# Optimization experiments

Measured on AMD Instinct MI355X. Metric: run time of the kernel, lower is better.

The kernel has to match this reference:

```python
import jax, jax.numpy as jnp
import numpy as np

N_NODES = 50000
EMBED_DIM = 100
N_RAND_EDGES = 600000
NEG_SLOPE = 0.2  # alpha in the original module


def _build_pairs(n_nodes, n_edges, seed=0):
    """Replicates: neighbors(v) = unique(out_nbrs(v) U in_nbrs(v)) for all v,
    flattened into (seg=v, nbr=u) pair arrays (symmetrized, deduped edge list)."""
    rng = np.random.default_rng(seed)
    src = rng.integers(0, n_nodes, n_edges)
    dst = rng.integers(0, n_nodes, n_edges)
    ring = np.arange(n_nodes)  # guarantee every node has a neighbor
    src = np.concatenate([src, ring])
    dst = np.concatenate([dst, (ring + 1) % n_nodes])
    seg = np.concatenate([src, dst])
    nbr = np.concatenate([dst, src])
    pairs = np.unique(np.stack([seg, nbr], axis=1), axis=0)  # sorted by seg
    return pairs[:, 0].astype(np.int32), pairs[:, 1].astype(np.int32)


def setup_inputs() -> dict:
    key = jax.random.key(0)
    k1, k2 = jax.random.split(key)
    hidden = jax.random.normal(k1, (N_NODES, EMBED_DIM), dtype=jnp.float32)
    # nn.Linear(embed_dim, 1, bias=False) weight, kaiming-uniform-ish scale
    W = jax.random.normal(k2, (EMBED_DIM,), dtype=jnp.float32) / np.sqrt(EMBED_DIM)
    seg_np, nbr_np = _build_pairs(N_NODES, N_RAND_EDGES)
    return {"hidden": hidden, "W": W,
            "seg": jnp.asarray(seg_np), "nbr": jnp.asarray(nbr_np)}


def reference(hidden, W, seg, nbr):
    n = hidden.shape[0]
    h_i = hidden[seg]            # [P, D] center node repeated per neighbor
    h_j = hidden[nbr]            # [P, D] gathered neighbor embeddings
    scores = jnp.einsum('pd,d->p', h_i * h_j, W)           # a(neighbors*hidden)
    scores = jnp.where(scores >= 0, scores, NEG_SLOPE * scores)  # leaky_relu
    # per-node (segment) softmax, numerically stable
    m = jax.ops.segment_max(scores, seg, num_segments=n)
    e = jnp.exp(scores - m[seg])
    z = jax.ops.segment_sum(e, seg, num_segments=n)
    alpha = e / z[seg]                                      # [P]
    out = jax.ops.segment_sum(alpha[:, None] * h_j, seg, num_segments=n)  # [N, D]
    return out
```

## Files before the change

### kernel.cpp

```cpp
#include <hip/hip_runtime.h>
#include <math.h>

#define D 100
#define NEG_SLOPE 0.2f
#define CHUNK 16
#define ROWU 52
#define NPB 2

#define COMPILER_FENCE() asm volatile("" ::: "memory")

typedef _Float16 f16x2 __attribute__((ext_vector_type(2)));
union U32H2 { unsigned int u; f16x2 h; };

__device__ __forceinline__ unsigned int pkh2(float x, float y) {
    U32H2 c; c.h.x = (_Float16)x; c.h.y = (_Float16)y; return c.u;
}

__device__ __forceinline__ float dot2u(unsigned int au, unsigned int xu, float acc) {
#if __has_builtin(__builtin_amdgcn_fdot2)
    U32H2 a, x; a.u = au; x.u = xu;
    return __builtin_amdgcn_fdot2(a.h, x.h, acc, false);
#else
    U32H2 a, x; a.u = au; x.u = xu;
    return acc + (float)a.h.x * (float)x.h.x + (float)a.h.y * (float)x.h.y;
#endif
}

template<int CTRL>
__device__ __forceinline__ float dppf(float x) {
    return __uint_as_float((unsigned)__builtin_amdgcn_update_dpp(
        0, (int)__float_as_uint(x), CTRL, 0xF, 0xF, true));
}
__device__ __forceinline__ float red16_max(float x) {
    x = fmaxf(x, dppf<0xB1>(x));
    x = fmaxf(x, dppf<0x4E>(x));
    x = fmaxf(x, dppf<0x124>(x));
    x = fmaxf(x, dppf<0x128>(x));
    return x;
}
__device__ __forceinline__ float red16_sum(float x) {
    x += dppf<0xB1>(x);
    x += dppf<0x4E>(x);
    x += dppf<0x124>(x);
    x += dppf<0x128>(x);
    return x;
}

__global__ void prep_kernel(const int* __restrict__ seg,
                            int* __restrict__ row_ptr,
                            const float* __restrict__ hidden,
                            unsigned int* __restrict__ hb,
                            int n, int P, int total25)
{
    int t = blockIdx.x * blockDim.x + threadIdx.x;
    if (t < P) {
        int s0 = seg[t];
        if (t == 0)
            for (int v = 0; v <= s0; v++) row_ptr[v] = 0;
        int s1 = (t + 1 < P) ? seg[t + 1] : n;
        for (int v = s0 + 1; v <= s1; v++) row_ptr[v] = t + 1;
    }
    if (t < total25) {
        int node = t / 25, k = t - node * 25;
        float4 f = ((const float4*)hidden)[t];
        *(uint2*)&hb[node * ROWU + 2 * k] =
            make_uint2(pkh2(f.x, f.y), pkh2(f.z, f.w));
    }
}

__launch_bounds__(64 * NPB, 8)
__global__ void gat_agg_kernel(const float* __restrict__ hidden,
                               const float* __restrict__ W,
                               const int* __restrict__ nbr,
                               const int* __restrict__ row_ptr,
                               const unsigned int* __restrict__ hb,
                               float* __restrict__ out,
                               int n, int P)
{
    __shared__ __align__(16) unsigned int s_hwp[NPB][ROWU];
    __shared__ __align__(16) unsigned int s_rows[NPB][CHUNK][ROWU];
    __shared__ __align__(16) float        s_e[NPB][CHUNK];

    const int lane = threadIdx.x & 63;
    const int wid  = threadIdx.x >> 6;
    const int v    = blockIdx.x * NPB + wid;
    if (v >= n) return;

    if (lane < 50) {
        float2 h2 = ((const float2*)(hidden + (long)v * D))[lane];
        float2 w2 = ((const float2*)W)[lane];
        s_hwp[wid][lane] = pkh2(h2.x * w2.x, h2.y * w2.y);
    }
    COMPILER_FENCE();

    const int start = row_ptr[v];
    const int end   = row_ptr[v + 1];

    if (end <= start) {
        if (lane < D / 2)
            ((float2*)(out + (long)v * D))[lane] = make_float2(0.f, 0.f);
        return;
    }

    const int q  = lane >> 4;
    const int jl = lane & 15;
    const int t0 = q * 3;

    const uint4* hwq = ((const uint4*)&s_hwp[wid][0]) + t0;
    const uint4 a0 = hwq[0], a1 = hwq[1], a2 = hwq[2];
    uint2 at = make_uint2(0u, 0u);
    if (q == 0) at = *(const uint2*)&s_hwp[wid][48];

    float m = -INFINITY, z = 0.f;
    float accx = 0.f, accy = 0.f;

    for (int c = start; c < end; c += CHUNK) {
        const int  cnt = min(CHUNK, end - c);
        const bool pv  = jl < cnt;

        const int nbv = pv ? nbr[c + jl] : 0;
        const uint4* row16 = ((const uint4*)hb) + nbv * (ROWU / 4) + t0;

        uint4 x0 = row16[0], x1 = row16[1], x2 = row16[2];
        uint2 xt = make_uint2(0u, 0u);
        if (q == 0) xt = *(const uint2*)&hb[nbv * ROWU + 48];

        float p0 = 0.f, p1 = 0.f, p2 = 0.f, p3 = 0.f;
        p0 = dot2u(a0.x, x0.x, p0);  p1 = dot2u(a0.y, x0.y, p1);
        p2 = dot2u(a0.z, x0.z, p2);  p3 = dot2u(a0.w, x0.w, p3);
        p0 = dot2u(a1.x, x1.x, p0);  p1 = dot2u(a1.y, x1.y, p1);
        p2 = dot2u(a1.z, x1.z, p2);  p3 = dot2u(a1.w, x1.w, p3);
        p0 = dot2u(a2.x, x2.x, p0);  p1 = dot2u(a2.y, x2.y, p1);
        p2 = dot2u(a2.z, x2.z, p2);  p3 = dot2u(a2.w, x2.w, p3);
        if (q == 0) {
            p0 = dot2u(at.x, xt.x, p0);
            p1 = dot2u(at.y, xt.y, p1);
        }

        uint4* dst16 = ((uint4*)&s_rows[wid][jl][0]) + t0;
        dst16[0] = x0; dst16[1] = x1; dst16[2] = x2;
        if (q == 0) *(uint2*)&s_rows[wid][jl][48] = xt;

        float part = (p0 + p1) + (p2 + p3);
        part += __shfl_xor(part, 16, 64);
        part += __shfl_xor(part, 32, 64);
        const float s = pv ? (part >= 0.f ? part : NEG_SLOPE * part)
                           : -INFINITY;

        const float m_new = fmaxf(m, red16_max(s));
        const float scale = __expf(m - m_new);
        const float e     = pv ? __expf(s - m_new) : 0.f;
        z = z * scale + red16_sum(e);
        accx *= scale; accy *= scale;

        if (lane < CHUNK) s_e[wid][lane] = e;
        COMPILER_FENCE();

        const int cnt4 = (cnt + 3) & ~3;
        if (lane < D / 2) {
            for (int j0 = 0; j0 < cnt4; j0 += 4) {
                const float4 ev = *(const float4*)&s_e[wid][j0];
                U32H2 u0, u1, u2, u3;
                u0.u = s_rows[wid][j0    ][lane];
                u1.u = s_rows[wid][j0 + 1][lane];
                u2.u = s_rows[wid][j0 + 2][lane];
                u3.u = s_rows[wid][j0 + 3][lane];
                accx = fmaf((float)u0.h.x, ev.x, accx);
                accy = fmaf((float)u0.h.y, ev.x, accy);
                accx = fmaf((float)u1.h.x, ev.y, accx);
                accy = fmaf((float)u1.h.y, ev.y, accy);
                accx = fmaf((float)u2.h.x, ev.z, accx);
                accy = fmaf((float)u2.h.y, ev.z, accy);
                accx = fmaf((float)u3.h.x, ev.w, accx);
                accy = fmaf((float)u3.h.y, ev.w, accy);
            }
        }
        COMPILER_FENCE();
        m = m_new;
    }

    if (lane < D / 2) {
        const float inv = 1.f / z;
        ((float2*)(out + (long)v * D))[lane] = make_float2(accx * inv, accy * inv);
    }
}

extern "C" void kernel_launch(void* const* d_in, const int* in_sizes, int n_in,
                              void* d_out, int out_size, void* d_ws, size_t ws_size,
                              hipStream_t stream) {
    const float* hidden = (const float*)d_in[0];
    const float* W      = (const float*)d_in[1];
    const int*   seg    = (const int*)d_in[2];
    const int*   nbr    = (const int*)d_in[3];
    float*       out    = (float*)d_out;

    const int Ddim = in_sizes[1];
    const int n    = in_sizes[0] / Ddim;
    const int P    = in_sizes[2];

    int* row_ptr = (int*)d_ws;
    size_t hb_off = (((size_t)(n + 1) * 4) + 255) & ~(size_t)255;
    unsigned int* hb = (unsigned int*)((char*)d_ws + hb_off);

    const int total25 = n * 25;
    const int tmax    = (P > total25) ? P : total25;
    hipLaunchKernelGGL(prep_kernel, dim3((tmax + 255) / 256), dim3(256), 0, stream,
                       seg, row_ptr, hidden, hb, n, P, total25);
    hipLaunchKernelGGL(gat_agg_kernel, dim3((n + NPB - 1) / NPB), dim3(64 * NPB),
                       0, stream, hidden, W, nbr, row_ptr, hb, out, n, P);
}
```

Measured before the change: 128.4 us.

## Accumulate weighted rows in registers per lane instead of staging through LDS

Each lane now keeps 28 per-column register accumulators for its own neighbor slice and multiplies them by its softmax weight directly. This removes the LDS staging of gathered rows and weights and the serial per-chunk accumulation loop. A DPP reduction across the 16 neighbor lanes runs once at the end, and the rescale is skipped when the running max does not change. The cost is higher register pressure (launch bound occupancy lowered from 8 to 6) and a final reduction of 28 values.

```diff
diff --git a/kernel.cpp b/kernel.cpp
--- a/kernel.cpp
+++ b/kernel.cpp
@@ -68,7 +68,19 @@
     }
 }
 
-__launch_bounds__(64 * NPB, 8)
+#define ACCU4(b, X) do {                                                      \
+    U32H2 t_;                                                                 \
+    t_.u = (X).x; accA[(b)+0] = fmaf((float)t_.h.x, e, accA[(b)+0]);          \
+                  accA[(b)+1] = fmaf((float)t_.h.y, e, accA[(b)+1]);          \
+    t_.u = (X).y; accA[(b)+2] = fmaf((float)t_.h.x, e, accA[(b)+2]);          \
+                  accA[(b)+3] = fmaf((float)t_.h.y, e, accA[(b)+3]);          \
+    t_.u = (X).z; accA[(b)+4] = fmaf((float)t_.h.x, e, accA[(b)+4]);          \
+                  accA[(b)+5] = fmaf((float)t_.h.y, e, accA[(b)+5]);          \
+    t_.u = (X).w; accA[(b)+6] = fmaf((float)t_.h.x, e, accA[(b)+6]);          \
+                  accA[(b)+7] = fmaf((float)t_.h.y, e, accA[(b)+7]);          \
+} while (0)
+
+__launch_bounds__(64 * NPB, 6)
 __global__ void gat_agg_kernel(const float* __restrict__ hidden,
                                const float* __restrict__ W,
                                const int* __restrict__ nbr,
@@ -78,8 +90,6 @@
                                int n, int P)
 {
     __shared__ __align__(16) unsigned int s_hwp[NPB][ROWU];
-    __shared__ __align__(16) unsigned int s_rows[NPB][CHUNK][ROWU];
-    __shared__ __align__(16) float        s_e[NPB][CHUNK];
 
     const int lane = threadIdx.x & 63;
     const int wid  = threadIdx.x >> 6;
@@ -111,8 +121,14 @@
     uint2 at = make_uint2(0u, 0u);
     if (q == 0) at = *(const uint2*)&s_hwp[wid][48];
 
+    float accA[24];
+    float accT[4];
+    #pragma unroll
+    for (int i = 0; i < 24; ++i) accA[i] = 0.f;
+    #pragma unroll
+    for (int i = 0; i < 4; ++i) accT[i] = 0.f;
+
     float m = -INFINITY, z = 0.f;
-    float accx = 0.f, accy = 0.f;
 
     for (int c = start; c < end; c += CHUNK) {
         const int  cnt = min(CHUNK, end - c);
@@ -137,10 +153,6 @@
             p1 = dot2u(at.y, xt.y, p1);
         }
 
-        uint4* dst16 = ((uint4*)&s_rows[wid][jl][0]) + t0;
-        dst16[0] = x0; dst16[1] = x1; dst16[2] = x2;
-        if (q == 0) *(uint2*)&s_rows[wid][jl][48] = xt;
-
         float part = (p0 + p1) + (p2 + p3);
         part += __shfl_xor(part, 16, 64);
         part += __shfl_xor(part, 32, 64);
@@ -148,41 +160,47 @@
                            : -INFINITY;
 
         const float m_new = fmaxf(m, red16_max(s));
-        const float scale = __expf(m - m_new);
         const float e     = pv ? __expf(s - m_new) : 0.f;
-        z = z * scale + red16_sum(e);
-        accx *= scale; accy *= scale;
-
-        if (lane < CHUNK) s_e[wid][lane] = e;
-        COMPILER_FENCE();
-
-        const int cnt4 = (cnt + 3) & ~3;
-        if (lane < D / 2) {
-            for (int j0 = 0; j0 < cnt4; j0 += 4) {
-                const float4 ev = *(const float4*)&s_e[wid][j0];
-                U32H2 u0, u1, u2, u3;
-                u0.u = s_rows[wid][j0    ][lane];
-                u1.u = s_rows[wid][j0 + 1][lane];
-                u2.u = s_rows[wid][j0 + 2][lane];
-                u3.u = s_rows[wid][j0 + 3][lane];
-                accx = fmaf((float)u0.h.x, ev.x, accx);
-                accy = fmaf((float)u0.h.y, ev.x, accy);
-                accx = fmaf((float)u1.h.x, ev.y, accx);
-                accy = fmaf((float)u1.h.y, ev.y, accy);
-                accx = fmaf((float)u2.h.x, ev.z, accx);
-                accy = fmaf((float)u2.h.y, ev.z, accy);
-                accx = fmaf((float)u3.h.x, ev.w, accx);
-                accy = fmaf((float)u3.h.y, ev.w, accy);
-            }
+        const float gsum  = red16_sum(e);
+
+        if (m_new != m) {
+            const float scale = __expf(m - m_new);
+            z *= scale;
+            #pragma unroll
+            for (int i = 0; i < 24; ++i) accA[i] *= scale;
+            #pragma unroll
+            for (int i = 0; i < 4; ++i) accT[i] *= scale;
+            m = m_new;
         }
-        COMPILER_FENCE();
-        m = m_new;
-    }
-
-    if (lane < D / 2) {
-        const float inv = 1.f / z;
-        ((float2*)(out + (long)v * D))[lane] = make_float2(accx * inv, accy * inv);
-    }
+        z += gsum;
+
+        ACCU4(0,  x0);
+        ACCU4(8,  x1);
+        ACCU4(16, x2);
+        if (q == 0) {
+            U32H2 t_;
+            t_.u = xt.x; accT[0] = fmaf((float)t_.h.x, e, accT[0]);
+                         accT[1] = fmaf((float)t_.h.y, e, accT[1]);
+            t_.u = xt.y; accT[2] = fmaf((float)t_.h.x, e, accT[2]);
+                         accT[3] = fmaf((float)t_.h.y, e, accT[3]);
+        }
+    }
+
+    #pragma unroll
+    for (int i = 0; i < 24; ++i) accA[i] = red16_sum(accA[i]);
+    #pragma unroll
+    for (int i = 0; i < 4; ++i) accT[i] = red16_sum(accT[i]);
+
+    const float inv = 1.f / z;
+    float2* orow = (float2*)(out + (long)v * D);
+    #pragma unroll
+    for (int j = 0; j < 12; ++j) {
+        if (jl == j)
+            orow[q * 12 + j] = make_float2(accA[2 * j] * inv,
+                                           accA[2 * j + 1] * inv);
+    }
+    if (lane == 12) orow[48] = make_float2(accT[0] * inv, accT[1] * inv);
+    if (lane == 13) orow[49] = make_float2(accT[2] * inv, accT[3] * inv);
 }
 
 extern "C" void kernel_launch(void* const* d_in, const int* in_sizes, int n_in,
```

New measurement: 141.4 us. 10.1% more time.
